# Performance work log

Measured on AMD Instinct MI355X. Metric: run time of the kernel, lower is better.

Reference implementation:

```python
import jax, jax.numpy as jnp
import numpy as np

B, C, T = 8, 256, 2048
DS = 4
SC = C // DS          # tsa_scale = 64
DEPTH = 256           # temporal_depth (band width)
BN_EPS = 1e-5


def _conv_bn_relu(x, W, b, g, beta, mu, var):
    # 1x1 conv on [B, C, T, 1] layout == channel matmul, then eval-mode BN, then ReLU
    y = jnp.einsum('bctz,oc->botz', x, W) + b[None, :, None, None]
    inv = g / jnp.sqrt(var + BN_EPS)
    y = (y - mu[None, :, None, None]) * inv[None, :, None, None] + beta[None, :, None, None]
    return jax.nn.relu(y)


def setup_inputs() -> dict:
    key = jax.random.key(0)
    ks = jax.random.split(key, 20)
    inp = {"x": jax.random.normal(ks[0], (B, C, T, 1), jnp.float32)}
    for name, oc, base in (("k", SC, 1), ("q", SC, 7), ("v", C, 13)):
        inp[name + "W"] = jax.random.normal(ks[base], (oc, C), jnp.float32) * 0.05
        inp[name + "b"] = jax.random.normal(ks[base + 1], (oc,), jnp.float32) * 0.05
        inp[name + "g"] = 1.0 + 0.05 * jax.random.normal(ks[base + 2], (oc,), jnp.float32)
        inp[name + "beta"] = jax.random.normal(ks[base + 3], (oc,), jnp.float32) * 0.05
        inp[name + "mu"] = jax.random.normal(ks[base + 4], (oc,), jnp.float32) * 0.05
        inp[name + "var"] = 1.0 + 0.1 * jax.random.uniform(ks[base + 5], (oc,), jnp.float32)
    return inp


def reference(x, kW, kb, kg, kbeta, kmu, kvar,
              qW, qb, qg, qbeta, qmu, qvar,
              vW, vb, vg, vbeta, vmu, vvar):
    key = _conv_bn_relu(x, kW, kb, kg, kbeta, kmu, kvar)[..., 0]                      # [B, SC, T]
    query = _conv_bn_relu(x, qW, qb, qg, qbeta, qmu, qvar)[..., 0].transpose(0, 2, 1)  # [B, T, SC]
    value = _conv_bn_relu(x, vW, vb, vg, vbeta, vmu, vvar)[..., 0].transpose(0, 2, 1)  # [B, T, C]

    i = jnp.arange(T)
    # tril(diag=0) * triu(diag=-(DEPTH-1)): causal band of width DEPTH
    mask = ((i[:, None] >= i[None, :]) & (i[:, None] - i[None, :] <= DEPTH - 1)).astype(x.dtype)

    s = jnp.einsum('btd,bds->bts', query, key) * mask / np.float32(np.sqrt(SC))
    s = jnp.exp(s - jnp.max(s, axis=2, keepdims=True)) * mask
    # NOTE: original torch code does `torch.sum(...)[0]`, indexing batch 0 of the
    # sum tensor ([T,1]) and broadcasting it across the batch. Replicated faithfully.
    s = s / (jnp.sum(s, axis=2, keepdims=True)[0] + 1e-30)

    tsa_out = jnp.einsum('bts,bsc->btc', s, value)                                     # [B, T, C]
    return x + tsa_out.transpose(0, 2, 1)[..., None]                                   # res_skip
```

## Files before the change

### kernel.cpp

```cpp
#include <hip/hip_runtime.h>

#define TDIM 2048

typedef __bf16 bf16_t;
typedef bf16_t bf16x8 __attribute__((ext_vector_type(8)));
typedef float f32x4 __attribute__((ext_vector_type(4)));
typedef unsigned short us8 __attribute__((ext_vector_type(8)));

__device__ __forceinline__ unsigned short f2bf(float x) {
  unsigned u = __builtin_bit_cast(unsigned, x);
  u += 0x7fffu + ((u >> 16) & 1u);
  return (unsigned short)(u >> 16);
}

__device__ __forceinline__ void gl_lds16(const unsigned short* g, unsigned short* l) {
  __builtin_amdgcn_global_load_lds(
      (const __attribute__((address_space(1))) unsigned int*)g,
      (__attribute__((address_space(3))) unsigned int*)l, 16, 0, 0);
}

__global__ __launch_bounds__(256) void k_prep(
    const float* __restrict__ x,
    const float* __restrict__ kW, const float* __restrict__ kb,
    const float* __restrict__ kg, const float* __restrict__ kbe,
    const float* __restrict__ kmu, const float* __restrict__ kva,
    const float* __restrict__ qW, const float* __restrict__ qb,
    const float* __restrict__ qg, const float* __restrict__ qbe,
    const float* __restrict__ qmu, const float* __restrict__ qva,
    const float* __restrict__ vW, const float* __restrict__ vb,
    const float* __restrict__ vg, const float* __restrict__ vbe,
    const float* __restrict__ vmu, const float* __restrict__ vva,
    unsigned short* __restrict__ xTf,
    unsigned short* __restrict__ effWf,
    float* __restrict__ effb)
{
  const int w = blockIdx.x;
  const int tid = threadIdx.x;

  if (w < 256) {
    const int tb = w & 31, b = w >> 5;
    const int t0 = tb * 64;
    __shared__ float Lf[64][66];
    for (int cc = 0; cc < 4; ++cc) {
      if (cc) __syncthreads();
#pragma unroll
      for (int pass = 0; pass < 4; ++pass) {
        int cl = pass * 16 + (tid >> 4);
        int tp = (tid & 15) * 4;
        float4 vx = *(const float4*)(x + (size_t)(b * 256 + cc * 64 + cl) * TDIM + t0 + tp);
        Lf[cl][tp] = vx.x; Lf[cl][tp + 1] = vx.y;
        Lf[cl][tp + 2] = vx.z; Lf[cl][tp + 3] = vx.w;
      }
      __syncthreads();
      unsigned short* dst = xTf + (((size_t)(b * 32 + tb) * 4 + cc) * 512) * 8;
#pragma unroll
      for (int pass = 0; pass < 2; ++pass) {
        int f = pass * 256 + tid;
        int nt = f >> 7, cblk = (f >> 4) & 7, m = f & 15;
        int t = nt * 16 + m;
        ushort4 lo, hi;
        lo.x = f2bf(Lf[cblk * 8 + 0][t]); lo.y = f2bf(Lf[cblk * 8 + 1][t]);
        lo.z = f2bf(Lf[cblk * 8 + 2][t]); lo.w = f2bf(Lf[cblk * 8 + 3][t]);
        hi.x = f2bf(Lf[cblk * 8 + 4][t]); hi.y = f2bf(Lf[cblk * 8 + 5][t]);
        hi.z = f2bf(Lf[cblk * 8 + 6][t]); hi.w = f2bf(Lf[cblk * 8 + 7][t]);
        *(ushort4*)(dst + f * 8) = lo;
        *(ushort4*)(dst + f * 8 + 4) = hi;
      }
    }
  } else {
    const int idx = w - 256;
    const int gid = idx >> 2, cc = idx & 3;
    unsigned short* dst = effWf + (size_t)idx * 1024 * 8;
#pragma unroll
    for (int pass = 0; pass < 4; ++pass) {
      int f = pass * 256 + tid;
      int ocblk = f >> 7, cblk = (f >> 4) & 7, m = f & 15;
      int G = gid * 128 + ocblk * 16 + m;
      const float* Wp = (G < 64) ? (kW + G * 256)
                       : (G < 128) ? (qW + (G - 64) * 256)
                                   : (vW + (G - 128) * 256);
      float gg = (G < 64) ? kg[G]  : (G < 128) ? qg[G - 64]  : vg[G - 128];
      float vr = (G < 64) ? kva[G] : (G < 128) ? qva[G - 64] : vva[G - 128];
      float inv = gg * rsqrtf(vr + 1e-5f);
      int c = cc * 64 + cblk * 8;
      float4 a = *(const float4*)(Wp + c);
      float4 bq = *(const float4*)(Wp + c + 4);
      ushort4 lo, hi;
      lo.x = f2bf(a.x * inv);  lo.y = f2bf(a.y * inv);
      lo.z = f2bf(a.z * inv);  lo.w = f2bf(a.w * inv);
      hi.x = f2bf(bq.x * inv); hi.y = f2bf(bq.y * inv);
      hi.z = f2bf(bq.z * inv); hi.w = f2bf(bq.w * inv);
      *(ushort4*)(dst + f * 8) = lo;
      *(ushort4*)(dst + f * 8 + 4) = hi;
    }
    if (idx == 0) {
      for (int G = tid; G < 384; G += 256) {
        float gg = (G < 64) ? kg[G]  : (G < 128) ? qg[G - 64]  : vg[G - 128];
        float vr = (G < 64) ? kva[G] : (G < 128) ? qva[G - 64] : vva[G - 128];
        float bb = (G < 64) ? kb[G]  : (G < 128) ? qb[G - 64]  : vb[G - 128];
        float mm = (G < 64) ? kmu[G] : (G < 128) ? qmu[G - 64] : vmu[G - 128];
        float be = (G < 64) ? kbe[G] : (G < 128) ? qbe[G - 64] : vbe[G - 128];
        float inv = gg * rsqrtf(vr + 1e-5f);
        effb[G] = (bb - mm) * inv + be;
      }
    }
  }
}

__global__ __launch_bounds__(256, 3) void k_qkv(
    const unsigned short* __restrict__ effWf,
    const float* __restrict__ effb,
    const unsigned short* __restrict__ xTf,
    unsigned short* __restrict__ vv,
    unsigned short* __restrict__ kT,
    unsigned short* __restrict__ qT)
{
  const int tb = blockIdx.x, gid = blockIdx.y, b = blockIdx.z;
  const int tid = threadIdx.x;
  const int lane = tid & 63, wv = tid >> 6;
  const int m = lane & 15, quad = lane >> 4;
  const int t0 = tb * 64;

  __shared__ unsigned short Wb[2][8192];
  __shared__ unsigned short Xb[2][4096];
  __shared__ float effbs[128];

  if (tid < 128) effbs[tid] = effb[gid * 128 + tid];

  const unsigned short* wbase = effWf + (size_t)gid * 4 * 1024 * 8;
  const unsigned short* xbase = xTf + ((size_t)(b * 32 + tb) * 4) * 512 * 8;

  auto stage = [&](int cc, int bufi) {
    const unsigned short* ws = wbase + (size_t)cc * 1024 * 8;
    const unsigned short* xs = xbase + (size_t)cc * 512 * 8;
#pragma unroll
    for (int i = 0; i < 4; ++i) {
      int ii = wv * 4 + i;
      gl_lds16(ws + (ii * 64 + lane) * 8, &Wb[bufi][ii * 512]);
    }
#pragma unroll
    for (int i = 0; i < 2; ++i) {
      int ii = wv * 2 + i;
      gl_lds16(xs + (ii * 64 + lane) * 8, &Xb[bufi][ii * 512]);
    }
  };

  const f32x4 fz = {0.f, 0.f, 0.f, 0.f};
  f32x4 acc[2][4];
#pragma unroll
  for (int i = 0; i < 2; ++i)
#pragma unroll
    for (int j = 0; j < 4; ++j) acc[i][j] = fz;

  stage(0, 0);
  for (int cc = 0; cc < 4; ++cc) {
    __syncthreads();
    if (cc < 3) stage(cc + 1, (cc + 1) & 1);
    const unsigned short* Wc = Wb[cc & 1];
    const unsigned short* Xc = Xb[cc & 1];
#pragma unroll
    for (int kk = 0; kk < 2; ++kk) {
      int cb = kk * 4 + quad;
      bf16x8 af[2], bfv[4];
#pragma unroll
      for (int mt = 0; mt < 2; ++mt)
        af[mt] = *(const bf16x8*)&Wc[(((wv * 2 + mt) * 8 + cb) * 16 + m) * 8];
#pragma unroll
      for (int nt = 0; nt < 4; ++nt)
        bfv[nt] = *(const bf16x8*)&Xc[((nt * 8 + cb) * 16 + m) * 8];
#pragma unroll
      for (int mt = 0; mt < 2; ++mt)
#pragma unroll
        for (int nt = 0; nt < 4; ++nt)
          acc[mt][nt] = __builtin_amdgcn_mfma_f32_16x16x32_bf16(af[mt], bfv[nt], acc[mt][nt], 0, 0, 0);
    }
  }

  if (gid == 0) {
#pragma unroll
    for (int mt = 0; mt < 2; ++mt)
#pragma unroll
      for (int nt = 0; nt < 4; ++nt) {
        int ocl = wv * 32 + mt * 16 + quad * 4;
        int t = t0 + nt * 16 + m;
        ushort4 s4;
        s4.x = f2bf(fmaxf(acc[mt][nt][0] + effbs[ocl + 0], 0.f));
        s4.y = f2bf(fmaxf(acc[mt][nt][1] + effbs[ocl + 1], 0.f));
        s4.z = f2bf(fmaxf(acc[mt][nt][2] + effbs[ocl + 2], 0.f));
        s4.w = f2bf(fmaxf(acc[mt][nt][3] + effbs[ocl + 3], 0.f));
        unsigned short* dst = (ocl < 64)
            ? (kT + ((size_t)(b * TDIM + t)) * 64 + ocl)
            : (qT + ((size_t)(b * TDIM + t)) * 64 + (ocl - 64));
        *(ushort4*)dst = s4;
      }
  } else {
#pragma unroll
    for (int mt = 0; mt < 2; ++mt)
#pragma unroll
      for (int nt = 0; nt < 4; ++nt)
#pragma unroll
        for (int r = 0; r < 4; ++r) {
          int ocl = wv * 32 + mt * 16 + quad * 4 + r;
          float y = fmaxf(acc[mt][nt][r] + effbs[ocl], 0.f);
          int c = (gid - 1) * 128 + ocl;
          int t = t0 + nt * 16 + m;
          vv[(size_t)(b * 256 + c) * TDIM + t] = f2bf(y);
        }
  }
}

__global__ __launch_bounds__(512, 1) void k_denom(
    const unsigned short* __restrict__ kT,
    const unsigned short* __restrict__ qT,
    float* __restrict__ denom0)
{
  const int t0d = blockIdx.x * 16;
  const int tid = threadIdx.x;
  const int lane = tid & 63, w = tid >> 6;
  const int m = lane & 15, quad = lane >> 4;

  __shared__ unsigned short Qs[16 * 64];
  __shared__ unsigned short Ks[272 * 64];
  __shared__ float pmaxs[8][16];
  __shared__ float psums[8][16];

  {
    const unsigned short* qg = qT + (size_t)t0d * 64;
#pragma unroll
    for (int it = 0; it < 5; ++it) {
      int idx = it * 512 + tid;
      if (idx < 2304) {
        int row = idx >> 3, dblk = idx & 7;
        us8 v = {0, 0, 0, 0, 0, 0, 0, 0};
        if (row < 16) {
          v = *(const us8*)(qg + row * 64 + dblk * 8);
          *(us8*)&Qs[row * 64 + ((dblk ^ (row & 7)) << 3)] = v;
        } else {
          int s = row - 16;
          int sg = t0d - 256 + s;
          if (sg >= 0) v = *(const us8*)(kT + (size_t)sg * 64 + dblk * 8);
          *(us8*)&Ks[s * 64 + ((dblk ^ (s & 7)) << 3)] = v;
        }
      }
    }
  }
  __syncthreads();

  const int jn = (w == 0) ? 3 : 2;
  f32x4 sc[3];
  {
    int t = m;
    bf16x8 qf0 = *(const bf16x8*)&Qs[t * 64 + ((quad ^ (t & 7)) << 3)];
    bf16x8 qf1 = *(const bf16x8*)&Qs[t * 64 + (((4 + quad) ^ (t & 7)) << 3)];
    const f32x4 fz = {0.f, 0.f, 0.f, 0.f};
#pragma unroll
    for (int jj = 0; jj < 3; ++jj) {
      if (jj < jn) {
        int j = w + jj * 8;
        int sr = 16 * j + m;
        f32x4 a = fz;
        bf16x8 kf0 = *(const bf16x8*)&Ks[sr * 64 + ((quad ^ (sr & 7)) << 3)];
        a = __builtin_amdgcn_mfma_f32_16x16x32_bf16(qf0, kf0, a, 0, 0, 0);
        bf16x8 kf1 = *(const bf16x8*)&Ks[sr * 64 + (((4 + quad) ^ (sr & 7)) << 3)];
        a = __builtin_amdgcn_mfma_f32_16x16x32_bf16(qf1, kf1, a, 0, 0, 0);
        sc[jj] = a;
      }
    }
  }

  float mx[4] = {0.f, 0.f, 0.f, 0.f};
#pragma unroll
  for (int jj = 0; jj < 3; ++jj)
    if (jj < jn) {
      int j = w + jj * 8;
#pragma unroll
      for (int r = 0; r < 4; ++r) {
        float v = sc[jj][r] * 0.125f;
        sc[jj][r] = v;
        int tg = t0d + quad * 4 + r;
        int sg = t0d - 256 + 16 * j + m;
        if (sg >= 0 && sg <= tg && tg - sg < 256) mx[r] = fmaxf(mx[r], v);
      }
    }
#pragma unroll
  for (int d = 1; d < 16; d <<= 1)
#pragma unroll
    for (int r = 0; r < 4; ++r) mx[r] = fmaxf(mx[r], __shfl_xor(mx[r], d, 64));
  if (m == 0)
#pragma unroll
    for (int r = 0; r < 4; ++r) pmaxs[w][quad * 4 + r] = mx[r];
  __syncthreads();

  float mxf[4];
#pragma unroll
  for (int r = 0; r < 4; ++r) {
    float v = pmaxs[0][quad * 4 + r];
#pragma unroll
    for (int ww = 1; ww < 8; ++ww) v = fmaxf(v, pmaxs[ww][quad * 4 + r]);
    mxf[r] = v;
  }
  float sm[4] = {0.f, 0.f, 0.f, 0.f};
#pragma unroll
  for (int jj = 0; jj < 3; ++jj)
    if (jj < jn) {
      int j = w + jj * 8;
#pragma unroll
      for (int r = 0; r < 4; ++r) {
        int tg = t0d + quad * 4 + r;
        int sg = t0d - 256 + 16 * j + m;
        if (sg >= 0 && sg <= tg && tg - sg < 256) sm[r] += __expf(sc[jj][r] - mxf[r]);
      }
    }
#pragma unroll
  for (int d = 1; d < 16; d <<= 1)
#pragma unroll
    for (int r = 0; r < 4; ++r) sm[r] += __shfl_xor(sm[r], d, 64);
  if (m == 0)
#pragma unroll
    for (int r = 0; r < 4; ++r) psums[w][quad * 4 + r] = sm[r];
  __syncthreads();

  if (tid < 16) {
    float s = 0.f;
#pragma unroll
    for (int ww = 0; ww < 8; ++ww) s += psums[ww][tid];
    denom0[t0d + tid] = s;
  }
}

__global__ __launch_bounds__(512, 4) void k_attn(
    const float* __restrict__ x,
    const unsigned short* __restrict__ vv,
    const unsigned short* __restrict__ kT,
    const unsigned short* __restrict__ qT,
    const float* __restrict__ denom0,
    float* __restrict__ out)
{
  const int tb = blockIdx.x, ch = blockIdx.y, b = blockIdx.z;
  const int tid = threadIdx.x;
  const int lane = tid & 63, w = tid >> 6;
  const int m = lane & 15, quad = lane >> 4;
  const int t0 = tb * 64;

  __shared__ unsigned short SM[24576];
  __shared__ float pmaxs[128];
  unsigned short* Qs = SM;
  unsigned short* Ks = SM + 4096;
  unsigned short* Ps = SM;

  {
    const unsigned short* qg  = qT + ((size_t)b * TDIM + t0) * 64;
    const unsigned short* kgb = kT + (size_t)b * TDIM * 64;
#pragma unroll
    for (int it = 0; it < 6; ++it) {
      int idx = it * 512 + tid;
      int row = idx >> 3, dblk = idx & 7;
      us8 v = {0, 0, 0, 0, 0, 0, 0, 0};
      if (row < 64) {
        v = *(const us8*)(qg + row * 64 + dblk * 8);
        *(us8*)&Qs[row * 64 + ((dblk ^ (row & 7)) << 3)] = v;
      } else {
        int s = row - 64;
        int sg = t0 - 256 + s;
        if (sg >= 0) v = *(const us8*)(kgb + (size_t)sg * 64 + dblk * 8);
        *(us8*)&Ks[s * 64 + ((dblk ^ (s & 7)) << 3)] = v;
      }
    }
  }
  __syncthreads();

  const int rt = w & 3, half = w >> 2;
  const int j0 = half ? 9 : 0;
  const int jn = half ? 8 : 9;
  f32x4 sc[9];
  {
    int t = rt * 16 + m;
    bf16x8 qf0 = *(const bf16x8*)&Qs[t * 64 + ((quad ^ (t & 7)) << 3)];
    bf16x8 qf1 = *(const bf16x8*)&Qs[t * 64 + (((4 + quad) ^ (t & 7)) << 3)];
    const f32x4 fz = {0.f, 0.f, 0.f, 0.f};
#pragma unroll
    for (int jj = 0; jj < 9; ++jj) {
      if (jj < jn) {
        int sr = 16 * (rt + j0 + jj) + m;
        f32x4 a = fz;
        bf16x8 kf0 = *(const bf16x8*)&Ks[sr * 64 + ((quad ^ (sr & 7)) << 3)];
        a = __builtin_amdgcn_mfma_f32_16x16x32_bf16(qf0, kf0, a, 0, 0, 0);
        bf16x8 kf1 = *(const bf16x8*)&Ks[sr * 64 + (((4 + quad) ^ (sr & 7)) << 3)];
        a = __builtin_amdgcn_mfma_f32_16x16x32_bf16(qf1, kf1, a, 0, 0, 0);
        sc[jj] = a;
      }
    }
  }

  const int tw = t0 + rt * 16;
  float mx[4] = {0.f, 0.f, 0.f, 0.f};
#pragma unroll
  for (int jj = 0; jj < 9; ++jj)
    if (jj < jn) {
#pragma unroll
      for (int r = 0; r < 4; ++r) {
        float v = sc[jj][r] * 0.125f;
        sc[jj][r] = v;
        int tg = tw + quad * 4 + r;
        int sg = t0 - 256 + 16 * (rt + j0 + jj) + m;
        if (sg >= 0 && sg <= tg && tg - sg < 256) mx[r] = fmaxf(mx[r], v);
      }
    }
#pragma unroll
  for (int d = 1; d < 16; d <<= 1)
#pragma unroll
    for (int r = 0; r < 4; ++r) mx[r] = fmaxf(mx[r], __shfl_xor(mx[r], d, 64));
  if (m == 0)
#pragma unroll
    for (int r = 0; r < 4; ++r) pmaxs[half * 64 + rt * 16 + quad * 4 + r] = mx[r];

  float dval[4];
#pragma unroll
  for (int r = 0; r < 4; ++r) dval[r] = denom0[tw + quad * 4 + r];

  __syncthreads();

  {
    us8 z = {0, 0, 0, 0, 0, 0, 0, 0};
#pragma unroll
    for (int it = 0; it < 6; ++it) {
      int idx = it * 512 + tid;
      if (idx < 2752) *(us8*)&Ps[idx * 8] = z;
    }
  }
  float mxf[4], rden[4];
#pragma unroll
  for (int r = 0; r < 4; ++r) {
    int row = rt * 16 + quad * 4 + r;
    mxf[r] = fmaxf(pmaxs[row], pmaxs[64 + row]);
    rden[r] = 1.f / (dval[r] + 1e-30f);
  }
#pragma unroll
  for (int jj = 0; jj < 9; ++jj)
    if (jj < jn) {
#pragma unroll
      for (int r = 0; r < 4; ++r) {
        int tg = tw + quad * 4 + r;
        int sg = t0 - 256 + 16 * (rt + j0 + jj) + m;
        bool ib = (sg >= 0 && sg <= tg && tg - sg < 256);
        sc[jj][r] = ib ? __expf(sc[jj][r] - mxf[r]) * rden[r] : 0.f;
      }
    }
  __syncthreads();

#pragma unroll
  for (int jj = 0; jj < 9; ++jj)
    if (jj < jn) {
      int col = 16 * (rt + j0 + jj) + m;
#pragma unroll
      for (int r = 0; r < 4; ++r)
        Ps[(rt * 16 + quad * 4 + r) * 344 + col] = f2bf(sc[jj][r]);
    }
  __syncthreads();

  const int cbase = ch * 128 + w * 16;
  const unsigned short* vrow = vv + (size_t)(b * 256 + cbase + m) * TDIM;
  const f32x4 fz = {0.f, 0.f, 0.f, 0.f};
  f32x4 acc[4] = {fz, fz, fz, fz};

  us8 vreg = {0, 0, 0, 0, 0, 0, 0, 0};
  if (t0 >= 256) vreg = *(const us8*)(vrow + t0 - 256 + quad * 8);
#pragma unroll
  for (int chunk = 0; chunk < 10; ++chunk) {
    us8 vnext = {0, 0, 0, 0, 0, 0, 0, 0};
    if (chunk < 9) {
      int sbase = t0 - 256 + (chunk + 1) * 32;
      if (sbase >= 0) vnext = *(const us8*)(vrow + sbase + quad * 8);
    }
    bf16x8 bfr = __builtin_bit_cast(bf16x8, vreg);
#pragma unroll
    for (int mt = 0; mt < 4; ++mt) {
      bf16x8 af = *(const bf16x8*)&Ps[(mt * 16 + m) * 344 + chunk * 32 + quad * 8];
      acc[mt] = __builtin_amdgcn_mfma_f32_16x16x32_bf16(af, bfr, acc[mt], 0, 0, 0);
    }
    vreg = vnext;
  }

#pragma unroll
  for (int mt = 0; mt < 4; ++mt) {
    int c = cbase + m;
    int t = t0 + mt * 16 + quad * 4;
    size_t off = (size_t)(b * 256 + c) * TDIM + t;
    float4 xv = *(const float4*)(x + off);
    float4 o;
    o.x = xv.x + acc[mt][0];
    o.y = xv.y + acc[mt][1];
    o.z = xv.z + acc[mt][2];
    o.w = xv.w + acc[mt][3];
    *(float4*)(out + off) = o;
  }
}

extern "C" void kernel_launch(void* const* d_in, const int* in_sizes, int n_in,
                              void* d_out, int out_size, void* d_ws, size_t ws_size,
                              hipStream_t stream) {
  const float* x   = (const float*)d_in[0];
  const float* kW  = (const float*)d_in[1];
  const float* kb  = (const float*)d_in[2];
  const float* kg  = (const float*)d_in[3];
  const float* kbe = (const float*)d_in[4];
  const float* kmu = (const float*)d_in[5];
  const float* kva = (const float*)d_in[6];
  const float* qW  = (const float*)d_in[7];
  const float* qb  = (const float*)d_in[8];
  const float* qg  = (const float*)d_in[9];
  const float* qbe = (const float*)d_in[10];
  const float* qmu = (const float*)d_in[11];
  const float* qva = (const float*)d_in[12];
  const float* vW  = (const float*)d_in[13];
  const float* vb  = (const float*)d_in[14];
  const float* vg  = (const float*)d_in[15];
  const float* vbe = (const float*)d_in[16];
  const float* vmu = (const float*)d_in[17];
  const float* vva = (const float*)d_in[18];

  unsigned short* vv  = (unsigned short*)d_ws;
  unsigned short* kTp = vv + (size_t)8 * 256 * TDIM;
  unsigned short* qTp = kTp + (size_t)8 * TDIM * 64;
  float* denom0 = (float*)(qTp + (size_t)8 * TDIM * 64);
  unsigned short* xTf = (unsigned short*)(denom0 + 2048);
  unsigned short* effWf = xTf + (size_t)8 * 256 * TDIM;
  float* effb = (float*)(effWf + 384 * 256);
  float* outp = (float*)d_out;

  k_prep<<<dim3(268), 256, 0, stream>>>(x,
      kW, kb, kg, kbe, kmu, kva,
      qW, qb, qg, qbe, qmu, qva,
      vW, vb, vg, vbe, vmu, vva, xTf, effWf, effb);
  k_qkv<<<dim3(32, 3, 8), 256, 0, stream>>>(effWf, effb, xTf, vv, kTp, qTp);
  k_denom<<<dim3(128), 512, 0, stream>>>(kTp, qTp, denom0);
  k_attn<<<dim3(32, 2, 8), 512, 0, stream>>>(x, vv, kTp, qTp, denom0, outp);
}
```

Before: 135.8 us.

## Fuse x transpose into QKV kernel and pre-swizzle K/Q for direct LDS loads

```diff
diff --git a/kernel.cpp b/kernel.cpp
--- a/kernel.cpp
+++ b/kernel.cpp
@@ -19,8 +19,7 @@
       (__attribute__((address_space(3))) unsigned int*)l, 16, 0, 0);
 }
 
-__global__ __launch_bounds__(256) void k_prep(
-    const float* __restrict__ x,
+__global__ __launch_bounds__(256) void k_prepw(
     const float* __restrict__ kW, const float* __restrict__ kb,
     const float* __restrict__ kg, const float* __restrict__ kbe,
     const float* __restrict__ kmu, const float* __restrict__ kva,
@@ -30,79 +29,44 @@
     const float* __restrict__ vW, const float* __restrict__ vb,
     const float* __restrict__ vg, const float* __restrict__ vbe,
     const float* __restrict__ vmu, const float* __restrict__ vva,
-    unsigned short* __restrict__ xTf,
     unsigned short* __restrict__ effWf,
     float* __restrict__ effb)
 {
-  const int w = blockIdx.x;
+  const int idx = blockIdx.x;
   const int tid = threadIdx.x;
-
-  if (w < 256) {
-    const int tb = w & 31, b = w >> 5;
-    const int t0 = tb * 64;
-    __shared__ float Lf[64][66];
-    for (int cc = 0; cc < 4; ++cc) {
-      if (cc) __syncthreads();
-#pragma unroll
-      for (int pass = 0; pass < 4; ++pass) {
-        int cl = pass * 16 + (tid >> 4);
-        int tp = (tid & 15) * 4;
-        float4 vx = *(const float4*)(x + (size_t)(b * 256 + cc * 64 + cl) * TDIM + t0 + tp);
-        Lf[cl][tp] = vx.x; Lf[cl][tp + 1] = vx.y;
-        Lf[cl][tp + 2] = vx.z; Lf[cl][tp + 3] = vx.w;
-      }
-      __syncthreads();
-      unsigned short* dst = xTf + (((size_t)(b * 32 + tb) * 4 + cc) * 512) * 8;
-#pragma unroll
-      for (int pass = 0; pass < 2; ++pass) {
-        int f = pass * 256 + tid;
-        int nt = f >> 7, cblk = (f >> 4) & 7, m = f & 15;
-        int t = nt * 16 + m;
-        ushort4 lo, hi;
-        lo.x = f2bf(Lf[cblk * 8 + 0][t]); lo.y = f2bf(Lf[cblk * 8 + 1][t]);
-        lo.z = f2bf(Lf[cblk * 8 + 2][t]); lo.w = f2bf(Lf[cblk * 8 + 3][t]);
-        hi.x = f2bf(Lf[cblk * 8 + 4][t]); hi.y = f2bf(Lf[cblk * 8 + 5][t]);
-        hi.z = f2bf(Lf[cblk * 8 + 6][t]); hi.w = f2bf(Lf[cblk * 8 + 7][t]);
-        *(ushort4*)(dst + f * 8) = lo;
-        *(ushort4*)(dst + f * 8 + 4) = hi;
-      }
-    }
-  } else {
-    const int idx = w - 256;
-    const int gid = idx >> 2, cc = idx & 3;
-    unsigned short* dst = effWf + (size_t)idx * 1024 * 8;
-#pragma unroll
-    for (int pass = 0; pass < 4; ++pass) {
-      int f = pass * 256 + tid;
-      int ocblk = f >> 7, cblk = (f >> 4) & 7, m = f & 15;
-      int G = gid * 128 + ocblk * 16 + m;
-      const float* Wp = (G < 64) ? (kW + G * 256)
-                       : (G < 128) ? (qW + (G - 64) * 256)
-                                   : (vW + (G - 128) * 256);
+  const int gid = idx >> 2, cc = idx & 3;
+  unsigned short* dst = effWf + (size_t)idx * 8192;
+#pragma unroll
+  for (int pass = 0; pass < 4; ++pass) {
+    int f = pass * 256 + tid;
+    int ocblk = f >> 7, cblk = (f >> 4) & 7, m = f & 15;
+    int G = gid * 128 + ocblk * 16 + m;
+    const float* Wp = (G < 64) ? (kW + G * 256)
+                     : (G < 128) ? (qW + (G - 64) * 256)
+                                 : (vW + (G - 128) * 256);
+    float gg = (G < 64) ? kg[G]  : (G < 128) ? qg[G - 64]  : vg[G - 128];
+    float vr = (G < 64) ? kva[G] : (G < 128) ? qva[G - 64] : vva[G - 128];
+    float inv = gg * rsqrtf(vr + 1e-5f);
+    int c = cc * 64 + cblk * 8;
+    float4 a = *(const float4*)(Wp + c);
+    float4 bq = *(const float4*)(Wp + c + 4);
+    ushort4 lo, hi;
+    lo.x = f2bf(a.x * inv);  lo.y = f2bf(a.y * inv);
+    lo.z = f2bf(a.z * inv);  lo.w = f2bf(a.w * inv);
+    hi.x = f2bf(bq.x * inv); hi.y = f2bf(bq.y * inv);
+    hi.z = f2bf(bq.z * inv); hi.w = f2bf(bq.w * inv);
+    *(ushort4*)(dst + f * 8) = lo;
+    *(ushort4*)(dst + f * 8 + 4) = hi;
+  }
+  if (idx == 0) {
+    for (int G = tid; G < 384; G += 256) {
       float gg = (G < 64) ? kg[G]  : (G < 128) ? qg[G - 64]  : vg[G - 128];
       float vr = (G < 64) ? kva[G] : (G < 128) ? qva[G - 64] : vva[G - 128];
+      float bb = (G < 64) ? kb[G]  : (G < 128) ? qb[G - 64]  : vb[G - 128];
+      float mm = (G < 64) ? kmu[G] : (G < 128) ? qmu[G - 64] : vmu[G - 128];
+      float be = (G < 64) ? kbe[G] : (G < 128) ? qbe[G - 64] : vbe[G - 128];
       float inv = gg * rsqrtf(vr + 1e-5f);
-      int c = cc * 64 + cblk * 8;
-      float4 a = *(const float4*)(Wp + c);
-      float4 bq = *(const float4*)(Wp + c + 4);
-      ushort4 lo, hi;
-      lo.x = f2bf(a.x * inv);  lo.y = f2bf(a.y * inv);
-      lo.z = f2bf(a.z * inv);  lo.w = f2bf(a.w * inv);
-      hi.x = f2bf(bq.x * inv); hi.y = f2bf(bq.y * inv);
-      hi.z = f2bf(bq.z * inv); hi.w = f2bf(bq.w * inv);
-      *(ushort4*)(dst + f * 8) = lo;
-      *(ushort4*)(dst + f * 8 + 4) = hi;
-    }
-    if (idx == 0) {
-      for (int G = tid; G < 384; G += 256) {
-        float gg = (G < 64) ? kg[G]  : (G < 128) ? qg[G - 64]  : vg[G - 128];
-        float vr = (G < 64) ? kva[G] : (G < 128) ? qva[G - 64] : vva[G - 128];
-        float bb = (G < 64) ? kb[G]  : (G < 128) ? qb[G - 64]  : vb[G - 128];
-        float mm = (G < 64) ? kmu[G] : (G < 128) ? qmu[G - 64] : vmu[G - 128];
-        float be = (G < 64) ? kbe[G] : (G < 128) ? qbe[G - 64] : vbe[G - 128];
-        float inv = gg * rsqrtf(vr + 1e-5f);
-        effb[G] = (bb - mm) * inv + be;
-      }
+      effb[G] = (bb - mm) * inv + be;
     }
   }
 }
@@ -110,10 +74,10 @@
 __global__ __launch_bounds__(256, 3) void k_qkv(
     const unsigned short* __restrict__ effWf,
     const float* __restrict__ effb,
-    const unsigned short* __restrict__ xTf,
+    const float* __restrict__ x,
     unsigned short* __restrict__ vv,
-    unsigned short* __restrict__ kT,
-    unsigned short* __restrict__ qT)
+    unsigned short* __restrict__ kTs,
+    unsigned short* __restrict__ qTs)
 {
   const int tb = blockIdx.x, gid = blockIdx.y, b = blockIdx.z;
   const int tid = threadIdx.x;
@@ -122,27 +86,32 @@
   const int t0 = tb * 64;
 
   __shared__ unsigned short Wb[2][8192];
-  __shared__ unsigned short Xb[2][4096];
+  __shared__ unsigned short Xs[4608];
   __shared__ float effbs[128];
 
   if (tid < 128) effbs[tid] = effb[gid * 128 + tid];
 
-  const unsigned short* wbase = effWf + (size_t)gid * 4 * 1024 * 8;
-  const unsigned short* xbase = xTf + ((size_t)(b * 32 + tb) * 4) * 512 * 8;
-
-  auto stage = [&](int cc, int bufi) {
-    const unsigned short* ws = wbase + (size_t)cc * 1024 * 8;
-    const unsigned short* xs = xbase + (size_t)cc * 512 * 8;
+  const unsigned short* wbase = effWf + (size_t)gid * 32768;
+  const float* xb = x + (size_t)b * 256 * TDIM + t0 + lane;
+
+  float xr[16];
+
+  auto stageW = [&](int cc, int bufi) {
+    const unsigned short* ws = wbase + cc * 8192;
 #pragma unroll
     for (int i = 0; i < 4; ++i) {
       int ii = wv * 4 + i;
       gl_lds16(ws + (ii * 64 + lane) * 8, &Wb[bufi][ii * 512]);
     }
-#pragma unroll
-    for (int i = 0; i < 2; ++i) {
-      int ii = wv * 2 + i;
-      gl_lds16(xs + (ii * 64 + lane) * 8, &Xb[bufi][ii * 512]);
-    }
+  };
+  auto loadX = [&](int cc) {
+#pragma unroll
+    for (int p = 0; p < 4; ++p)
+#pragma unroll
+      for (int j = 0; j < 4; ++j) {
+        int c = cc * 64 + p * 16 + wv * 4 + j;
+        xr[p * 4 + j] = xb[(size_t)c * TDIM];
+      }
   };
 
   const f32x4 fz = {0.f, 0.f, 0.f, 0.f};
@@ -152,12 +121,22 @@
 #pragma unroll
     for (int j = 0; j < 4; ++j) acc[i][j] = fz;
 
-  stage(0, 0);
+  stageW(0, 0);
+  loadX(0);
   for (int cc = 0; cc < 4; ++cc) {
     __syncthreads();
-    if (cc < 3) stage(cc + 1, (cc + 1) & 1);
+#pragma unroll
+    for (int p = 0; p < 4; ++p) {
+      int cb4 = p * 16 + wv * 4;
+      int swz = (((cb4 >> 3) ^ (lane >> 3)) << 3) | (cb4 & 7);
+      ushort4 s4;
+      s4.x = f2bf(xr[p * 4 + 0]); s4.y = f2bf(xr[p * 4 + 1]);
+      s4.z = f2bf(xr[p * 4 + 2]); s4.w = f2bf(xr[p * 4 + 3]);
+      *(ushort4*)&Xs[lane * 72 + swz] = s4;
+    }
+    if (cc < 3) { stageW(cc + 1, (cc + 1) & 1); loadX(cc + 1); }
+    __syncthreads();
     const unsigned short* Wc = Wb[cc & 1];
-    const unsigned short* Xc = Xb[cc & 1];
 #pragma unroll
     for (int kk = 0; kk < 2; ++kk) {
       int cb = kk * 4 + quad;
@@ -166,8 +145,10 @@
       for (int mt = 0; mt < 2; ++mt)
         af[mt] = *(const bf16x8*)&Wc[(((wv * 2 + mt) * 8 + cb) * 16 + m) * 8];
 #pragma unroll
-      for (int nt = 0; nt < 4; ++nt)
-        bfv[nt] = *(const bf16x8*)&Xc[((nt * 8 + cb) * 16 + m) * 8];
+      for (int nt = 0; nt < 4; ++nt) {
+        int t = nt * 16 + m;
+        bfv[nt] = *(const bf16x8*)&Xs[t * 72 + ((cb ^ (t >> 3)) << 3)];
+      }
 #pragma unroll
       for (int mt = 0; mt < 2; ++mt)
 #pragma unroll
@@ -188,10 +169,14 @@
         s4.y = f2bf(fmaxf(acc[mt][nt][1] + effbs[ocl + 1], 0.f));
         s4.z = f2bf(fmaxf(acc[mt][nt][2] + effbs[ocl + 2], 0.f));
         s4.w = f2bf(fmaxf(acc[mt][nt][3] + effbs[ocl + 3], 0.f));
-        unsigned short* dst = (ocl < 64)
-            ? (kT + ((size_t)(b * TDIM + t)) * 64 + ocl)
-            : (qT + ((size_t)(b * TDIM + t)) * 64 + (ocl - 64));
-        *(ushort4*)dst = s4;
+        if (ocl < 64) {
+          int col = (((ocl >> 3) ^ (t & 7)) << 3) | (ocl & 7);
+          *(ushort4*)(kTs + ((size_t)(b * TDIM + t)) * 64 + col) = s4;
+        } else {
+          int oq = ocl - 64;
+          int col = (((oq >> 3) ^ (t & 7)) << 3) | (oq & 7);
+          *(ushort4*)(qTs + ((size_t)(b * TDIM + t)) * 64 + col) = s4;
+        }
       }
   } else {
 #pragma unroll
@@ -210,8 +195,8 @@
 }
 
 __global__ __launch_bounds__(512, 1) void k_denom(
-    const unsigned short* __restrict__ kT,
-    const unsigned short* __restrict__ qT,
+    const unsigned short* __restrict__ kTs,
+    const unsigned short* __restrict__ qTs,
     float* __restrict__ denom0)
 {
   const int t0d = blockIdx.x * 16;
@@ -219,28 +204,21 @@
   const int lane = tid & 63, w = tid >> 6;
   const int m = lane & 15, quad = lane >> 4;
 
-  __shared__ unsigned short Qs[16 * 64];
-  __shared__ unsigned short Ks[272 * 64];
+  __shared__ unsigned short S[18432];
+  unsigned short* Qs = S;
+  unsigned short* Ks = S + 1024;
   __shared__ float pmaxs[8][16];
   __shared__ float psums[8][16];
 
   {
-    const unsigned short* qg = qT + (size_t)t0d * 64;
+    const unsigned short* qg = qTs + (size_t)t0d * 64;
+    const unsigned short* kg = kTs + ((long)t0d - 256) * 64;
 #pragma unroll
     for (int it = 0; it < 5; ++it) {
-      int idx = it * 512 + tid;
-      if (idx < 2304) {
-        int row = idx >> 3, dblk = idx & 7;
-        us8 v = {0, 0, 0, 0, 0, 0, 0, 0};
-        if (row < 16) {
-          v = *(const us8*)(qg + row * 64 + dblk * 8);
-          *(us8*)&Qs[row * 64 + ((dblk ^ (row & 7)) << 3)] = v;
-        } else {
-          int s = row - 16;
-          int sg = t0d - 256 + s;
-          if (sg >= 0) v = *(const us8*)(kT + (size_t)sg * 64 + dblk * 8);
-          *(us8*)&Ks[s * 64 + ((dblk ^ (s & 7)) << 3)] = v;
-        }
+      int j = it * 512 + tid;
+      if (j < 2304) {
+        const unsigned short* g = (j < 128) ? (qg + j * 8) : (kg + (size_t)(j - 128) * 8);
+        gl_lds16(g, &S[(it * 512 + w * 64) * 8]);
       }
     }
   }
@@ -331,8 +309,8 @@
 __global__ __launch_bounds__(512, 4) void k_attn(
     const float* __restrict__ x,
     const unsigned short* __restrict__ vv,
-    const unsigned short* __restrict__ kT,
-    const unsigned short* __restrict__ qT,
+    const unsigned short* __restrict__ kTs,
+    const unsigned short* __restrict__ qTs,
     const float* __restrict__ denom0,
     float* __restrict__ out)
 {
@@ -349,27 +327,23 @@
   unsigned short* Ps = SM;
 
   {
-    const unsigned short* qg  = qT + ((size_t)b * TDIM + t0) * 64;
-    const unsigned short* kgb = kT + (size_t)b * TDIM * 64;
+    const unsigned short* qg = qTs + ((size_t)(b * TDIM + t0)) * 64;
+    const unsigned short* kg = kTs + ((long)(b * TDIM + t0) - 256) * 64;
 #pragma unroll
     for (int it = 0; it < 6; ++it) {
-      int idx = it * 512 + tid;
-      int row = idx >> 3, dblk = idx & 7;
-      us8 v = {0, 0, 0, 0, 0, 0, 0, 0};
-      if (row < 64) {
-        v = *(const us8*)(qg + row * 64 + dblk * 8);
-        *(us8*)&Qs[row * 64 + ((dblk ^ (row & 7)) << 3)] = v;
-      } else {
-        int s = row - 64;
-        int sg = t0 - 256 + s;
-        if (sg >= 0) v = *(const us8*)(kgb + (size_t)sg * 64 + dblk * 8);
-        *(us8*)&Ks[s * 64 + ((dblk ^ (s & 7)) << 3)] = v;
-      }
-    }
-  }
+      int j = it * 512 + tid;
+      const unsigned short* g = (j < 512) ? (qg + (size_t)j * 8)
+                                          : (kg + (size_t)(j - 512) * 8);
+      gl_lds16(g, &SM[(it * 512 + w * 64) * 8]);
+    }
+  }
+  const int rt = w & 3, half = w >> 2;
+  const int tw = t0 + rt * 16;
+  float dval[4];
+#pragma unroll
+  for (int r = 0; r < 4; ++r) dval[r] = denom0[tw + quad * 4 + r];
   __syncthreads();
 
-  const int rt = w & 3, half = w >> 2;
   const int j0 = half ? 9 : 0;
   const int jn = half ? 8 : 9;
   f32x4 sc[9];
@@ -392,7 +366,6 @@
     }
   }
 
-  const int tw = t0 + rt * 16;
   float mx[4] = {0.f, 0.f, 0.f, 0.f};
 #pragma unroll
   for (int jj = 0; jj < 9; ++jj)
@@ -414,20 +387,8 @@
 #pragma unroll
     for (int r = 0; r < 4; ++r) pmaxs[half * 64 + rt * 16 + quad * 4 + r] = mx[r];
 
-  float dval[4];
-#pragma unroll
-  for (int r = 0; r < 4; ++r) dval[r] = denom0[tw + quad * 4 + r];
-
   __syncthreads();
 
-  {
-    us8 z = {0, 0, 0, 0, 0, 0, 0, 0};
-#pragma unroll
-    for (int it = 0; it < 6; ++it) {
-      int idx = it * 512 + tid;
-      if (idx < 2752) *(us8*)&Ps[idx * 8] = z;
-    }
-  }
   float mxf[4], rden[4];
 #pragma unroll
   for (int r = 0; r < 4; ++r) {
@@ -446,8 +407,20 @@
         sc[jj][r] = ib ? __expf(sc[jj][r] - mxf[r]) * rden[r] : 0.f;
       }
     }
-  __syncthreads();
-
+
+  if (half == 0) {
+    if (rt > 0) {
+      int row = rt * 16 + (lane >> 2), col = 16 * rt - 16 + (lane & 3) * 4;
+      ushort4 z; z.x = 0; z.y = 0; z.z = 0; z.w = 0;
+      *(ushort4*)&Ps[row * 344 + col] = z;
+    }
+  } else {
+    if (rt < 3) {
+      int row = rt * 16 + (lane >> 2), col = 16 * rt + 272 + (lane & 3) * 4;
+      ushort4 z; z.x = 0; z.y = 0; z.z = 0; z.w = 0;
+      *(ushort4*)&Ps[row * 344 + col] = z;
+    }
+  }
 #pragma unroll
   for (int jj = 0; jj < 9; ++jj)
     if (jj < jn) {
@@ -456,15 +429,16 @@
       for (int r = 0; r < 4; ++r)
         Ps[(rt * 16 + quad * 4 + r) * 344 + col] = f2bf(sc[jj][r]);
     }
-  __syncthreads();
 
   const int cbase = ch * 128 + w * 16;
   const unsigned short* vrow = vv + (size_t)(b * 256 + cbase + m) * TDIM;
+  us8 vreg = {0, 0, 0, 0, 0, 0, 0, 0};
+  if (t0 >= 256) vreg = *(const us8*)(vrow + t0 - 256 + quad * 8);
+
+  __syncthreads();
+
   const f32x4 fz = {0.f, 0.f, 0.f, 0.f};
   f32x4 acc[4] = {fz, fz, fz, fz};
-
-  us8 vreg = {0, 0, 0, 0, 0, 0, 0, 0};
-  if (t0 >= 256) vreg = *(const us8*)(vrow + t0 - 256 + quad * 8);
 #pragma unroll
   for (int chunk = 0; chunk < 10; ++chunk) {
     us8 vnext = {0, 0, 0, 0, 0, 0, 0, 0};
@@ -475,8 +449,11 @@
     bf16x8 bfr = __builtin_bit_cast(bf16x8, vreg);
 #pragma unroll
     for (int mt = 0; mt < 4; ++mt) {
-      bf16x8 af = *(const bf16x8*)&Ps[(mt * 16 + m) * 344 + chunk * 32 + quad * 8];
-      acc[mt] = __builtin_amdgcn_mfma_f32_16x16x32_bf16(af, bfr, acc[mt], 0, 0, 0);
+      const int cs = mt >> 1;
+      if (chunk >= cs && chunk <= cs + 8) {
+        bf16x8 af = *(const bf16x8*)&Ps[(mt * 16 + m) * 344 + chunk * 32 + quad * 8];
+        acc[mt] = __builtin_amdgcn_mfma_f32_16x16x32_bf16(af, bfr, acc[mt], 0, 0, 0);
+      }
     }
     vreg = vnext;
   }
@@ -520,19 +497,18 @@
   const float* vva = (const float*)d_in[18];
 
   unsigned short* vv  = (unsigned short*)d_ws;
-  unsigned short* kTp = vv + (size_t)8 * 256 * TDIM;
-  unsigned short* qTp = kTp + (size_t)8 * TDIM * 64;
-  float* denom0 = (float*)(qTp + (size_t)8 * TDIM * 64);
-  unsigned short* xTf = (unsigned short*)(denom0 + 2048);
-  unsigned short* effWf = xTf + (size_t)8 * 256 * TDIM;
-  float* effb = (float*)(effWf + 384 * 256);
+  unsigned short* kTs = vv + (size_t)8 * 256 * TDIM;
+  unsigned short* qTs = kTs + (size_t)8 * TDIM * 64;
+  float* denom0 = (float*)(qTs + (size_t)8 * TDIM * 64);
+  unsigned short* effWf = (unsigned short*)(denom0 + 2048);
+  float* effb = (float*)(effWf + 12 * 8192);
   float* outp = (float*)d_out;
 
-  k_prep<<<dim3(268), 256, 0, stream>>>(x,
+  k_prepw<<<dim3(12), 256, 0, stream>>>(
       kW, kb, kg, kbe, kmu, kva,
       qW, qb, qg, qbe, qmu, qva,
-      vW, vb, vg, vbe, vmu, vva, xTf, effWf, effb);
-  k_qkv<<<dim3(32, 3, 8), 256, 0, stream>>>(effWf, effb, xTf, vv, kTp, qTp);
-  k_denom<<<dim3(128), 512, 0, stream>>>(kTp, qTp, denom0);
-  k_attn<<<dim3(32, 2, 8), 512, 0, stream>>>(x, vv, kTp, qTp, denom0, outp);
-}
+      vW, vb, vg, vbe, vmu, vva, effWf, effb);
+  k_qkv<<<dim3(32, 3, 8), 256, 0, stream>>>(effWf, effb, x, vv, kTs, qTs);
+  k_denom<<<dim3(128), 512, 0, stream>>>(kTs, qTs, denom0);
+  k_attn<<<dim3(32, 2, 8), 512, 0, stream>>>(x, vv, kTs, qTs, denom0, outp);
+}
```

Measured after the change: 133.7 us. Within noise of the previous version (-1.6%).
